# Optimization experiments

Hardware: AMD Instinct MI355X
Metric: run time of the kernel (lower is better)

The kernel has to match this reference:

```python
import jax, jax.numpy as jnp
import numpy as np

RADIUS = 2
TOP_K = 4096
TEMPERATURE = 0.1
KSIZE = 2 * RADIUS + 1  # 5


def _max_pool(x, r):
    k = 2 * r + 1
    return jax.lax.reduce_window(x, -jnp.inf, jax.lax.max,
                                 (1, 1, k, k), (1, 1, 1, 1), 'SAME')


def simple_nms(scores, r):
    zeros = jnp.zeros_like(scores)
    max_mask = scores == _max_pool(scores, r)
    for _ in range(2):
        supp_mask = _max_pool(max_mask.astype(scores.dtype), r) > 0
        supp_scores = jnp.where(supp_mask, zeros, scores)
        new_max_mask = supp_scores == _max_pool(supp_scores, r)
        max_mask = max_mask | (new_max_mask & ~supp_mask)
    return jnp.where(max_mask, scores, zeros)


def _bilinear_sample(img, px, py):
    # grid_sample, mode=bilinear, padding_mode=zeros, align_corners=True.
    # img: [H, W]; px, py: pixel coords [K]
    H, W = img.shape
    x0 = jnp.floor(px); y0 = jnp.floor(py)
    wx1 = px - x0; wx0 = 1.0 - wx1
    wy1 = py - y0; wy0 = 1.0 - wy1

    def g(xf, yf):
        xi = jnp.clip(xf.astype(jnp.int32), 0, W - 1)
        yi = jnp.clip(yf.astype(jnp.int32), 0, H - 1)
        valid = (xf >= 0) & (xf <= W - 1) & (yf >= 0) & (yf <= H - 1)
        return jnp.where(valid, img[yi, xi], 0.0)

    return (wy0 * wx0 * g(x0, y0) + wy0 * wx1 * g(x0 + 1, y0)
            + wy1 * wx0 * g(x0, y0 + 1) + wy1 * wx1 * g(x0 + 1, y0 + 1))


def setup_inputs() -> dict:
    key = jax.random.key(0)
    scores_map = jax.random.uniform(key, (8, 1, 1024, 1024), dtype=jnp.float32)
    return {'scores_map': scores_map}


def reference(scores_map):
    b, c, H, W = scores_map.shape
    r = RADIUS

    scores_nograd = jax.lax.stop_gradient(scores_map)
    nms = simple_nms(scores_nograd, r)
    # zero the borders (image_size is None)
    nms = nms.at[:, :, :r, :].set(0.0)
    nms = nms.at[:, :, :, :r].set(0.0)
    nms = nms.at[:, :, -r:, :].set(0.0)
    nms = nms.at[:, :, :, -r:].set(0.0)

    # top_k > 0 branch: fixed-size selection per image
    _, idx = jax.lax.top_k(nms.reshape(b, -1), TOP_K)  # [B, K]
    rows = idx // W
    cols = idx % W

    # soft-argmax offset grid: (dx, dy) pairs, row-major over the 5x5 patch
    lin = jnp.linspace(-r, r, KSIZE, dtype=scores_map.dtype)
    gi, gj = jnp.meshgrid(lin, lin, indexing='ij')
    hw_grid = jnp.stack([gj.reshape(-1), gi.reshape(-1)], axis=-1)  # [25, 2]

    # gather 5x5 patches at keypoints (equivalent to unfold + row-index)
    oi, oj = jnp.meshgrid(jnp.arange(KSIZE), jnp.arange(KSIZE), indexing='ij')
    oi = oi.reshape(-1); oj = oj.reshape(-1)  # [25]
    padded = jnp.pad(scores_map[:, 0], ((0, 0), (r, r), (r, r)))  # zero pad like Unfold

    def gather_patches(pad_s, rr, cc):
        return pad_s[rr[:, None] + oi[None, :], cc[:, None] + oj[None, :]]  # [K, 25]

    patches = jax.vmap(gather_patches)(padded, rows, cols)  # [B, K, 25]

    max_v = jax.lax.stop_gradient(patches.max(axis=-1, keepdims=True))
    x_exp = jnp.exp((patches - max_v) / TEMPERATURE)  # [B, K, 25]
    ssum = x_exp.sum(axis=-1)  # [B, K]
    xy_residual = jnp.einsum('bkp,pc->bkc', x_exp, hw_grid) / ssum[..., None]

    diff = (hw_grid[None, None, :, :] - xy_residual[:, :, None, :]) / r
    hw_grid_dist2 = jnp.sum(diff * diff, axis=-1)  # [B, K, 25]
    scoredispersity = jnp.sum(x_exp * hw_grid_dist2, axis=-1) / ssum  # [B, K]

    kpts_nms = jnp.stack([cols, rows], axis=-1).astype(scores_map.dtype)  # (x, y)
    wh = jnp.array([W - 1, H - 1], dtype=scores_map.dtype)
    keypoints_xy = (kpts_nms + xy_residual) / wh * 2.0 - 1.0  # [B, K, 2] in [-1, 1]

    # grid_sample lookup of the (differentiable) score map at sub-pixel locations
    px = (keypoints_xy[..., 0] + 1.0) * 0.5 * (W - 1)
    py = (keypoints_xy[..., 1] + 1.0) * 0.5 * (H - 1)
    kptscores = jax.vmap(_bilinear_sample)(scores_map[:, 0], px, py)  # [B, K]

    return keypoints_xy, scoredispersity, kptscores
```

## Files before the change

kernel.cpp:

```cpp
#include <hip/hip_runtime.h>

typedef unsigned int u32;
typedef unsigned long long u64;

#define B 8
#define H 1024
#define W 1024
#define TOPK 4096
#define CANDCAP 131072
#define GCAP 8192
#define LBUFW 320
#define CSTR 32
#define NB2 8192
#define HPAD 8200
#define BAND 4096

#define MAX5R(A, j) fmaxf(fmaxf(fmaxf(A[j], A[(j)+1]), fmaxf(A[(j)+2], A[(j)+3])), A[(j)+4])
#define OR5(A, j) (A[j] | A[(j)+1] | A[(j)+2] | A[(j)+3] | A[(j)+4])

__device__ __forceinline__ u32 bkt(u32 vb) {
    if (vb < 0x3F000000u) return 0u;
    u32 b = ((vb - 0x3F000000u) >> 10) + 1u;
    return b > NB2 ? NB2 : b;
}

__device__ __forceinline__ u64 xdilate(u64 m) {
    return m | (m << 1) | (m >> 1) | (m << 2) | (m >> 2);
}

__device__ __forceinline__ float xmax5(float v) {
    float a = fmaxf(fmaxf(__shfl_up(v, 1), __shfl_down(v, 1)), v);
    return fmaxf(a, fmaxf(__shfl_up(v, 2), __shfl_down(v, 2)));
}

__device__ __forceinline__ float selz(u64 m, float v) {
    float r;
    asm("v_cndmask_b32 %0, %1, 0, %2" : "=v"(r) : "v"(v), "s"(m));
    return r;
}
__device__ __forceinline__ float selnz(u64 m, float v) {
    float r;
    asm("v_cndmask_b32 %0, 0, %1, %2" : "=v"(r) : "v"(v), "s"(m));
    return r;
}


__global__ __launch_bounds__(256, 4) void k_nms(const float* __restrict__ S_,
                                                u64* __restrict__ cand,
                                                u32* __restrict__ cnt) {
    __shared__ u64 lbuf[4][LBUFW];

    int lane = threadIdx.x & 63;
    int wslot = threadIdx.x >> 6;
    int sx = blockIdx.x * 4 + wslot;
    int sy = blockIdx.y;
    int img = blockIdx.z;
    int gx0 = sx * 44 - 10;
    int gy0 = sy * 32;
    int gx = gx0 + lane;
    bool lxok = (unsigned)gx < (unsigned)W;
    u64 lanebit = 1ull << lane;
    const float* Sb = S_ + ((size_t)img << 20);

    u64 validx = __ballot(lxok);
    u64 emask = __ballot(lane >= 10 && lane <= 53 && gx >= 2 && gx <= W - 3);

    float S[14], R0[8], R1[8], R2[8], nxt[4];
    u64 M0[8], M1[8], SP1[6], SP2[6];
#pragma unroll
    for (int k = 0; k < 14; ++k) S[k] = -1.0f;
#pragma unroll
    for (int k = 0; k < 8; ++k) { R0[k] = -1e30f; R1[k] = -1e30f; R2[k] = -1e30f; M0[k] = 0; M1[k] = 0; }
#pragma unroll
    for (int k = 0; k < 6; ++k) { SP1[k] = 0; SP2[k] = 0; }

    u32 wbase = 0;
    int y0 = gy0 - 10;

#pragma unroll
    for (int j = 0; j < 4; ++j) {
        int gy = y0 + j;
        nxt[j] = ((unsigned)gy < (unsigned)H && lxok) ? Sb[(gy << 10) + gx] : -1.0f;
    }

    for (int cy = 0; cy < 13; ++cy, y0 += 4) {
#pragma unroll
        for (int j = 0; j < 4; ++j) S[10 + j] = nxt[j];
        if (cy < 12) {
#pragma unroll
            for (int j = 0; j < 4; ++j) {
                int gy = y0 + 4 + j;
                nxt[j] = ((unsigned)gy < (unsigned)H && lxok) ? Sb[(gy << 10) + gx] : -1.0f;
            }
        }
#pragma unroll
        for (int j = 0; j < 4; ++j) {
            R0[4 + j] = xmax5(S[10 + j]);
            float c0 = MAX5R(R0, j);
            u64 m0 = __ballot(S[j + 8] == c0) & validx;
            M0[4 + j] = m0;

            u64 sp1 = xdilate(OR5(M0, j));
            SP1[2 + j] = sp1;

            float ss1 = selz(sp1, S[j + 6]);
            R1[4 + j] = xmax5(ss1);
            float c1 = MAX5R(R1, j);
            float ss1b = selz(SP1[j], S[j + 4]);
            u64 new1 = __ballot(ss1b == c1) & validx;
            u64 m1 = M0[j] | (new1 & ~SP1[j]);
            M1[4 + j] = m1;

            u64 sp2 = xdilate(OR5(M1, j));
            SP2[2 + j] = sp2;

            float ss2 = selz(sp2, S[j + 2]);
            R2[4 + j] = xmax5(ss2);

            if (cy >= 5) {
                float c2 = MAX5R(R2, j);
                float ss2b = selz(SP2[j], S[j]);
                u64 new2 = __ballot(ss2b == c2) & validx;
                u64 m2 = M1[j] | (new2 & ~SP2[j]);
                int gy_out = y0 + j - 10;
                if (gy_out >= 2 && gy_out <= H - 3) {
                    float val = selnz(m2, S[j]);
                    u64 bm = __ballot(val > 0.0f) & emask;
                    if (bm) {
                        u32 cw = (u32)__popcll(bm);
                        u32 prefix = (u32)__popcll(bm & (lanebit - 1ull));
                        if ((bm & lanebit) && (wbase + prefix) < LBUFW) {
                            u64 key = (((u64)__float_as_uint(val)) << 32) |
                                      (u32)(~(u32)((gy_out << 10) + gx));
                            lbuf[wslot][wbase + prefix] = key;
                        }
                        wbase += cw;
                    }
                }
            }
        }
#pragma unroll
        for (int k = 0; k < 10; ++k) S[k] = S[k + 4];
#pragma unroll
        for (int k = 0; k < 4; ++k) {
            R0[k] = R0[k + 4]; R1[k] = R1[k + 4]; R2[k] = R2[k + 4];
            M0[k] = M0[k + 4]; M1[k] = M1[k + 4];
        }
#pragma unroll
        for (int k = 0; k < 2; ++k) { SP1[k] = SP1[k + 4]; SP2[k] = SP2[k + 4]; }
    }

    u32 total = wbase > LBUFW ? LBUFW : wbase;
    u32 gbase = 0;
    if (lane == 0) gbase = atomicAdd(&cnt[img * CSTR], total);
    gbase = (u32)__shfl((int)gbase, 0, 64);
    u64* dst = cand + ((size_t)img << 17);
    for (u32 i = lane; i < total; i += 64)
        dst[gbase + i] = lbuf[wslot][i];
}


__global__ __launch_bounds__(256) void k_hist(const u64* __restrict__ cand,
                                              const u32* __restrict__ cnt,
                                              u32* __restrict__ hist) {
    __shared__ u32 h[NB2 + 1];
    int img = blockIdx.y;
    int t = threadIdx.x;
    for (int i = t; i <= NB2; i += 256) h[i] = 0;
    __syncthreads();
    u32 n = cnt[img * CSTR];
    if (n > CANDCAP) n = CANDCAP;
    const u64* c = cand + ((size_t)img << 17);
    u32 per = (n + gridDim.x - 1) / gridDim.x;
    u32 lo = blockIdx.x * per;
    u32 hiX = lo + per; if (hiX > n) hiX = n;
    for (u32 i = lo + t; i < hiX; i += 256)
        atomicAdd(&h[bkt((u32)(c[i] >> 32))], 1u);
    __syncthreads();
    u32* gh = hist + (u32)img * HPAD;
    for (int i = t; i <= NB2; i += 256)
        if (h[i]) atomicAdd(&gh[i], h[i]);
}


__global__ __launch_bounds__(1024) void k_scan(const u32* __restrict__ hist,
                                               u32* __restrict__ dparr,
                                               u32* __restrict__ dpcnt,
                                               u32* __restrict__ Bsr,
                                               u32* __restrict__ gtot) {
    __shared__ u32 wpart[16], woff[16];
    __shared__ u32 sBs, sGc;
    int img = blockIdx.x, t = threadIdx.x;
    int lane = t & 63, wid = t >> 6;
    const u32* h = hist + (u32)img * HPAD;
    int hi = NB2 - 8 * t;
    u32 loc[8];
    u32 psum = 0;
#pragma unroll
    for (int i = 0; i < 8; ++i) { loc[i] = h[hi - i]; psum += loc[i]; }
    u32 incl = psum;
#pragma unroll
    for (int d = 1; d < 64; d <<= 1) {
        u32 x = (u32)__shfl_up((int)incl, d);
        if (lane >= d) incl += x;
    }
    if (lane == 63) wpart[wid] = incl;
    if (t == 0) { sBs = 0; sGc = 0; }
    __syncthreads();
    if (t == 0) { u32 a = 0; for (int w2 = 0; w2 < 16; ++w2) { woff[w2] = a; a += wpart[w2]; } }
    __syncthreads();
    u32 total1 = woff[15] + wpart[15];
    u32 excl = incl - psum + woff[wid];

    u32* dpi = dparr + (u32)img * HPAD;
    u32* dci = dpcnt + (u32)img * HPAD;
    u32 dpv = excl;
#pragma unroll
    for (int i = 0; i < 8; ++i) {
        dpi[hi - i] = dpv;
        dci[hi - i] = dpv;
        dpv += loc[i];
    }
    if (t == 1023) { dpi[0] = dpv; dci[0] = dpv; }
    if (excl < TOPK && excl + psum >= TOPK) {
        u32 cum = excl;
#pragma unroll
        for (int i = 0; i < 8; ++i) {
            cum += loc[i];
            if (cum >= TOPK) { sBs = (u32)(hi - i); sGc = cum; break; }
        }
    }
    __syncthreads();
    if (t == 0) {
        u32 bs = sBs, gc = sGc;
        if (total1 < TOPK) { bs = 0; gc = total1 + h[0]; }
        Bsr[img * CSTR] = bs;
        gtot[img * CSTR] = gc > GCAP ? GCAP : gc;
    }
}


__global__ __launch_bounds__(256) void k_gather(const u64* __restrict__ cand,
                                                const u32* __restrict__ cnt,
                                                const u32* __restrict__ Bsr,
                                                u32* __restrict__ dpcnt,
                                                u64* __restrict__ gath) {
    __shared__ u32 hb[BAND];
    __shared__ u32 ho[BAND];
    int img = blockIdx.y, t = threadIdx.x;
    for (int i = t; i < BAND; i += 256) hb[i] = 0;
    __syncthreads();
    u32 n = cnt[img * CSTR];
    if (n > CANDCAP) n = CANDCAP;
    u32 Bs = Bsr[img * CSTR];
    const u64* c = cand + ((size_t)img << 17);
    u32* dci = dpcnt + (u32)img * HPAD;
    u32 per = (n + gridDim.x - 1) / gridDim.x;
    u32 lo = blockIdx.x * per;
    u32 hiX = lo + per; if (hiX > n) hiX = n;

    for (u32 i = lo + t; i < hiX; i += 256) {
        u32 b = bkt((u32)(c[i] >> 32));
        if (b >= Bs) {
            u32 idx = b - Bs;
            if (idx < BAND) atomicAdd(&hb[idx], 1u);
        }
    }
    __syncthreads();
    for (int i = t; i < BAND; i += 256) {
        u32 cv = hb[i];
        if (cv) { ho[i] = atomicAdd(&dci[Bs + i], cv); hb[i] = 0; }
    }
    __syncthreads();
    u64* g = gath + ((size_t)img << 13);
    for (u32 i = lo + t; i < hiX; i += 256) {
        u64 key = c[i];
        u32 b = bkt((u32)(key >> 32));
        if (b < Bs) continue;
        u32 idx = b - Bs;
        u32 pos;
        if (idx < BAND) pos = ho[idx] + atomicAdd(&hb[idx], 1u);
        else pos = atomicAdd(&dci[b], 1u);
        if (pos < GCAP) g[pos] = key;
    }
}


__global__ __launch_bounds__(256) void k_rankfinal(const u64* __restrict__ gath,
                                                   const u32* __restrict__ gtot,
                                                   const u32* __restrict__ dparr,
                                                   const float* __restrict__ S,
                                                   float* __restrict__ out) {
    int img = blockIdx.y;
    u32 n = gtot[img * CSTR];
    if (n > GCAP) n = GCAP;
    u32 i = blockIdx.x * 256 + threadIdx.x;
    if (i >= n) return;
    const u64* g = gath + ((size_t)img << 13);
    u64 key = g[i];
    u32 b = bkt((u32)(key >> 32));
    const u32* dpi = dparr + (u32)img * HPAD;
    u32 lo = dpi[b];
    u32 hiE = (b >= 1) ? dpi[b - 1] : n;
    if (hiE > n) hiE = n;
    u32 r = lo;
    for (u32 j = lo; j < hiE; ++j) r += (g[j] > key);
    if (r >= TOPK) return;

    u32 rem = ~(u32)(key & 0xFFFFFFFFull);
    int row = (int)(rem >> 10);
    int col = (int)(rem & (W - 1));
    const float* Sb = S + ((size_t)img << 20);

    float p[25];
    float mx = -1e30f;
#pragma unroll
    for (int a2 = 0; a2 < 5; ++a2) {
        int y = row + a2 - 2;
#pragma unroll
        for (int c2 = 0; c2 < 5; ++c2) {
            int x = col + c2 - 2;
            float v = (y >= 0 && y < H && x >= 0 && x < W) ? Sb[(y << 10) + x] : 0.0f;
            p[a2 * 5 + c2] = v;
            mx = fmaxf(mx, v);
        }
    }
    float sum = 0.0f, sx = 0.0f, sy = 0.0f;
#pragma unroll
    for (int a2 = 0; a2 < 5; ++a2) {
#pragma unroll
        for (int c2 = 0; c2 < 5; ++c2) {
            float e = expf((p[a2 * 5 + c2] - mx) / 0.1f);
            p[a2 * 5 + c2] = e;
            sum += e;
            sx += e * (float)(c2 - 2);
            sy += e * (float)(a2 - 2);
        }
    }
    float rx = sx / sum, ry = sy / sum;
    float sd = 0.0f;
#pragma unroll
    for (int a2 = 0; a2 < 5; ++a2) {
#pragma unroll
        for (int c2 = 0; c2 < 5; ++c2) {
            float dxx = ((float)(c2 - 2) - rx) * 0.5f;
            float dyy = ((float)(a2 - 2) - ry) * 0.5f;
            sd += p[a2 * 5 + c2] * (dxx * dxx + dyy * dyy);
        }
    }
    float disp = sd / sum;
    float kx = ((float)col + rx) / (float)(W - 1) * 2.0f - 1.0f;
    float ky = ((float)row + ry) / (float)(H - 1) * 2.0f - 1.0f;

    float px = (kx + 1.0f) * 0.5f * (float)(W - 1);
    float py = (ky + 1.0f) * 0.5f * (float)(H - 1);
    float x0 = floorf(px), y0 = floorf(py);
    float wx1 = px - x0, wx0 = 1.0f - wx1;
    float wy1 = py - y0, wy0 = 1.0f - wy1;

    float gg[4];
    float xs[4] = {x0, x0 + 1.0f, x0, x0 + 1.0f};
    float ys[4] = {y0, y0, y0 + 1.0f, y0 + 1.0f};
#pragma unroll
    for (int q = 0; q < 4; ++q) {
        int xi = (int)xs[q]; xi = xi < 0 ? 0 : (xi > W - 1 ? W - 1 : xi);
        int yi = (int)ys[q]; yi = yi < 0 ? 0 : (yi > H - 1 ? H - 1 : yi);
        bool valid = (xs[q] >= 0.0f) && (xs[q] <= (float)(W - 1)) &&
                     (ys[q] >= 0.0f) && (ys[q] <= (float)(H - 1));
        gg[q] = valid ? Sb[(yi << 10) + xi] : 0.0f;
    }
    float score = wy0 * wx0 * gg[0] + wy0 * wx1 * gg[1] + wy1 * wx0 * gg[2] + wy1 * wx1 * gg[3];

    u32 slot = ((u32)img << 12) + r;
    out[(size_t)slot * 2]     = kx;
    out[(size_t)slot * 2 + 1] = ky;
    out[B * TOPK * 2 + slot]            = disp;
    out[B * TOPK * 2 + B * TOPK + slot] = score;
}


extern "C" void kernel_launch(void* const* d_in, const int* in_sizes, int n_in,
                              void* d_out, int out_size, void* d_ws, size_t ws_size,
                              hipStream_t stream) {
    const float* S = (const float*)d_in[0];
    float* out = (float*)d_out;

    char* w = (char*)d_ws;
    u64* cand = (u64*)w;        w += (size_t)B * CANDCAP * 8;
    u64* gath = (u64*)w;        w += (size_t)B * GCAP * 8;
    u32* hist = (u32*)w;        w += (size_t)B * HPAD * 4;
    u32* cnt = (u32*)w;         w += B * CSTR * 4;
    u32* dparr = (u32*)w;       w += (size_t)B * HPAD * 4;
    u32* dpcnt = (u32*)w;       w += (size_t)B * HPAD * 4;
    u32* Bsr = (u32*)w;         w += B * CSTR * 4;
    u32* gtot = (u32*)w;        w += B * CSTR * 4;

    hipMemsetAsync(hist, 0, (size_t)B * HPAD * 4 + B * CSTR * 4, stream);

    k_nms<<<dim3(6, 32, B), 256, 0, stream>>>(S, cand, cnt);
    k_hist<<<dim3(16, B), 256, 0, stream>>>(cand, cnt, hist);
    k_scan<<<B, 1024, 0, stream>>>(hist, dparr, dpcnt, Bsr, gtot);
    k_gather<<<dim3(16, B), 256, 0, stream>>>(cand, cnt, Bsr, dpcnt, gath);
    k_rankfinal<<<dim3(32, B), 256, 0, stream>>>(gath, gtot, dparr, S, out);
}
```

Before: 114.5 us.

## Fuse histogram into NMS kernel, coarsen buckets, reuse row shuffles across NMS passes

Builds the per-image score histogram inside the NMS kernel from the local candidate buffer, which removes the separate histogram kernel and its second pass over the candidate array. Bucket resolution drops from 8192 to 1024 bins, so scan, gather and shared-memory histograms get simpler and no longer need a global-atomic fallback outside the band. The horizontal max-of-5 now caches the shifted neighbour values once per row and reuses them with masked selects in the suppression passes, replacing repeated cross-lane shuffles. The cost is more registers in the NMS kernel, a shared histogram plus a barrier there, and coarser buckets that may pass more candidates into the threshold band.

```diff
diff --git a/kernel.cpp b/kernel.cpp
--- a/kernel.cpp
+++ b/kernel.cpp
@@ -11,26 +11,24 @@
 #define GCAP 8192
 #define LBUFW 320
 #define CSTR 32
-#define NB2 8192
-#define HPAD 8200
-#define BAND 4096
+#define NB 1024
+#define HPAD 1056
 
 #define MAX5R(A, j) fmaxf(fmaxf(fmaxf(A[j], A[(j)+1]), fmaxf(A[(j)+2], A[(j)+3])), A[(j)+4])
 #define OR5(A, j) (A[j] | A[(j)+1] | A[(j)+2] | A[(j)+3] | A[(j)+4])
 
 __device__ __forceinline__ u32 bkt(u32 vb) {
     if (vb < 0x3F000000u) return 0u;
-    u32 b = ((vb - 0x3F000000u) >> 10) + 1u;
-    return b > NB2 ? NB2 : b;
+    u32 b = ((vb - 0x3F000000u) >> 13) + 1u;
+    return b > NB ? NB : b;
+}
+
+__device__ __forceinline__ float max5(float a, float b, float c, float d, float e) {
+    return fmaxf(fmaxf(fmaxf(a, b), fmaxf(c, d)), e);
 }
 
 __device__ __forceinline__ u64 xdilate(u64 m) {
     return m | (m << 1) | (m >> 1) | (m << 2) | (m >> 2);
-}
-
-__device__ __forceinline__ float xmax5(float v) {
-    float a = fmaxf(fmaxf(__shfl_up(v, 1), __shfl_down(v, 1)), v);
-    return fmaxf(a, fmaxf(__shfl_up(v, 2), __shfl_down(v, 2)));
 }
 
 __device__ __forceinline__ float selz(u64 m, float v) {
@@ -47,8 +45,10 @@
 
 __global__ __launch_bounds__(256, 4) void k_nms(const float* __restrict__ S_,
                                                 u64* __restrict__ cand,
-                                                u32* __restrict__ cnt) {
+                                                u32* __restrict__ cnt,
+                                                u32* __restrict__ hist) {
     __shared__ u64 lbuf[4][LBUFW];
+    __shared__ u32 bh[NB + 1];
 
     int lane = threadIdx.x & 63;
     int wslot = threadIdx.x >> 6;
@@ -62,13 +62,17 @@
     u64 lanebit = 1ull << lane;
     const float* Sb = S_ + ((size_t)img << 20);
 
+    for (int i = threadIdx.x; i <= NB; i += 256) bh[i] = 0;
+
     u64 validx = __ballot(lxok);
     u64 emask = __ballot(lane >= 10 && lane <= 53 && gx >= 2 && gx <= W - 3);
 
-    float S[14], R0[8], R1[8], R2[8], nxt[4];
+    float S[14], U1[12], U2[12], D1[12], D2[12], R0[8], R1[8], R2[8], nxt[4];
     u64 M0[8], M1[8], SP1[6], SP2[6];
 #pragma unroll
     for (int k = 0; k < 14; ++k) S[k] = -1.0f;
+#pragma unroll
+    for (int k = 0; k < 12; ++k) { U1[k] = -1.0f; U2[k] = -1.0f; D1[k] = -1.0f; D2[k] = -1.0f; }
 #pragma unroll
     for (int k = 0; k < 8; ++k) { R0[k] = -1e30f; R1[k] = -1e30f; R2[k] = -1e30f; M0[k] = 0; M1[k] = 0; }
 #pragma unroll
@@ -95,7 +99,13 @@
         }
 #pragma unroll
         for (int j = 0; j < 4; ++j) {
-            R0[4 + j] = xmax5(S[10 + j]);
+            float v = S[10 + j];
+            U1[8 + j] = __shfl_up(v, 1);
+            U2[8 + j] = __shfl_up(v, 2);
+            D1[8 + j] = __shfl_down(v, 1);
+            D2[8 + j] = __shfl_down(v, 2);
+
+            R0[4 + j] = max5(U2[8 + j], U1[8 + j], v, D1[8 + j], D2[8 + j]);
             float c0 = MAX5R(R0, j);
             u64 m0 = __ballot(S[j + 8] == c0) & validx;
             M0[4 + j] = m0;
@@ -103,8 +113,10 @@
             u64 sp1 = xdilate(OR5(M0, j));
             SP1[2 + j] = sp1;
 
-            float ss1 = selz(sp1, S[j + 6]);
-            R1[4 + j] = xmax5(ss1);
+            float h1 = max5(selz(sp1 << 2, U2[j + 4]), selz(sp1 << 1, U1[j + 4]),
+                            selz(sp1, S[j + 6]),
+                            selz(sp1 >> 1, D1[j + 4]), selz(sp1 >> 2, D2[j + 4]));
+            R1[4 + j] = h1;
             float c1 = MAX5R(R1, j);
             float ss1b = selz(SP1[j], S[j + 4]);
             u64 new1 = __ballot(ss1b == c1) & validx;
@@ -114,8 +126,10 @@
             u64 sp2 = xdilate(OR5(M1, j));
             SP2[2 + j] = sp2;
 
-            float ss2 = selz(sp2, S[j + 2]);
-            R2[4 + j] = xmax5(ss2);
+            float h2 = max5(selz(sp2 << 2, U2[j]), selz(sp2 << 1, U1[j]),
+                            selz(sp2, S[j + 2]),
+                            selz(sp2 >> 1, D1[j]), selz(sp2 >> 2, D2[j]));
+            R2[4 + j] = h2;
 
             if (cy >= 5) {
                 float c2 = MAX5R(R2, j);
@@ -142,6 +156,8 @@
 #pragma unroll
         for (int k = 0; k < 10; ++k) S[k] = S[k + 4];
 #pragma unroll
+        for (int k = 0; k < 8; ++k) { U1[k] = U1[k + 4]; U2[k] = U2[k + 4]; D1[k] = D1[k + 4]; D2[k] = D2[k + 4]; }
+#pragma unroll
         for (int k = 0; k < 4; ++k) {
             R0[k] = R0[k + 4]; R1[k] = R1[k + 4]; R2[k] = R2[k + 4];
             M0[k] = M0[k + 4]; M1[k] = M1[k + 4];
@@ -155,31 +171,15 @@
     if (lane == 0) gbase = atomicAdd(&cnt[img * CSTR], total);
     gbase = (u32)__shfl((int)gbase, 0, 64);
     u64* dst = cand + ((size_t)img << 17);
-    for (u32 i = lane; i < total; i += 64)
-        dst[gbase + i] = lbuf[wslot][i];
-}
-
-
-__global__ __launch_bounds__(256) void k_hist(const u64* __restrict__ cand,
-                                              const u32* __restrict__ cnt,
-                                              u32* __restrict__ hist) {
-    __shared__ u32 h[NB2 + 1];
-    int img = blockIdx.y;
-    int t = threadIdx.x;
-    for (int i = t; i <= NB2; i += 256) h[i] = 0;
-    __syncthreads();
-    u32 n = cnt[img * CSTR];
-    if (n > CANDCAP) n = CANDCAP;
-    const u64* c = cand + ((size_t)img << 17);
-    u32 per = (n + gridDim.x - 1) / gridDim.x;
-    u32 lo = blockIdx.x * per;
-    u32 hiX = lo + per; if (hiX > n) hiX = n;
-    for (u32 i = lo + t; i < hiX; i += 256)
-        atomicAdd(&h[bkt((u32)(c[i] >> 32))], 1u);
+    for (u32 i = lane; i < total; i += 64) {
+        u64 key = lbuf[wslot][i];
+        dst[gbase + i] = key;
+        atomicAdd(&bh[bkt((u32)(key >> 32))], 1u);
+    }
     __syncthreads();
     u32* gh = hist + (u32)img * HPAD;
-    for (int i = t; i <= NB2; i += 256)
-        if (h[i]) atomicAdd(&gh[i], h[i]);
+    for (int i = threadIdx.x; i <= NB; i += 256)
+        if (bh[i]) atomicAdd(&gh[i], bh[i]);
 }
 
 
@@ -193,12 +193,8 @@
     int img = blockIdx.x, t = threadIdx.x;
     int lane = t & 63, wid = t >> 6;
     const u32* h = hist + (u32)img * HPAD;
-    int hi = NB2 - 8 * t;
-    u32 loc[8];
-    u32 psum = 0;
-#pragma unroll
-    for (int i = 0; i < 8; ++i) { loc[i] = h[hi - i]; psum += loc[i]; }
-    u32 incl = psum;
+    u32 v = h[NB - t];
+    u32 incl = v;
 #pragma unroll
     for (int d = 1; d < 64; d <<= 1) {
         u32 x = (u32)__shfl_up((int)incl, d);
@@ -209,31 +205,19 @@
     __syncthreads();
     if (t == 0) { u32 a = 0; for (int w2 = 0; w2 < 16; ++w2) { woff[w2] = a; a += wpart[w2]; } }
     __syncthreads();
-    u32 total1 = woff[15] + wpart[15];
-    u32 excl = incl - psum + woff[wid];
-
+    u32 cum = incl + woff[wid];
+    u32 total = woff[15] + wpart[15];
+    u32 dp = cum - v;
     u32* dpi = dparr + (u32)img * HPAD;
     u32* dci = dpcnt + (u32)img * HPAD;
-    u32 dpv = excl;
-#pragma unroll
-    for (int i = 0; i < 8; ++i) {
-        dpi[hi - i] = dpv;
-        dci[hi - i] = dpv;
-        dpv += loc[i];
-    }
-    if (t == 1023) { dpi[0] = dpv; dci[0] = dpv; }
-    if (excl < TOPK && excl + psum >= TOPK) {
-        u32 cum = excl;
-#pragma unroll
-        for (int i = 0; i < 8; ++i) {
-            cum += loc[i];
-            if (cum >= TOPK) { sBs = (u32)(hi - i); sGc = cum; break; }
-        }
-    }
+    dpi[NB - t] = dp;
+    dci[NB - t] = dp;
+    if (t == 1023) { dpi[0] = cum; dci[0] = cum; }
+    if (total >= TOPK && dp < TOPK && cum >= TOPK) { sBs = (u32)(NB - t); sGc = cum; }
     __syncthreads();
     if (t == 0) {
         u32 bs = sBs, gc = sGc;
-        if (total1 < TOPK) { bs = 0; gc = total1 + h[0]; }
+        if (total < TOPK) { bs = 0; gc = total + h[0]; }
         Bsr[img * CSTR] = bs;
         gtot[img * CSTR] = gc > GCAP ? GCAP : gc;
     }
@@ -245,10 +229,10 @@
                                                 const u32* __restrict__ Bsr,
                                                 u32* __restrict__ dpcnt,
                                                 u64* __restrict__ gath) {
-    __shared__ u32 hb[BAND];
-    __shared__ u32 ho[BAND];
+    __shared__ u32 hb[NB + 1];
+    __shared__ u32 ho[NB + 1];
     int img = blockIdx.y, t = threadIdx.x;
-    for (int i = t; i < BAND; i += 256) hb[i] = 0;
+    for (int i = t; i <= NB; i += 256) hb[i] = 0;
     __syncthreads();
     u32 n = cnt[img * CSTR];
     if (n > CANDCAP) n = CANDCAP;
@@ -261,13 +245,10 @@
 
     for (u32 i = lo + t; i < hiX; i += 256) {
         u32 b = bkt((u32)(c[i] >> 32));
-        if (b >= Bs) {
-            u32 idx = b - Bs;
-            if (idx < BAND) atomicAdd(&hb[idx], 1u);
-        }
-    }
-    __syncthreads();
-    for (int i = t; i < BAND; i += 256) {
+        if (b >= Bs) atomicAdd(&hb[b - Bs], 1u);
+    }
+    __syncthreads();
+    for (int i = t; i <= NB; i += 256) {
         u32 cv = hb[i];
         if (cv) { ho[i] = atomicAdd(&dci[Bs + i], cv); hb[i] = 0; }
     }
@@ -278,9 +259,7 @@
         u32 b = bkt((u32)(key >> 32));
         if (b < Bs) continue;
         u32 idx = b - Bs;
-        u32 pos;
-        if (idx < BAND) pos = ho[idx] + atomicAdd(&hb[idx], 1u);
-        else pos = atomicAdd(&dci[b], 1u);
+        u32 pos = ho[idx] + atomicAdd(&hb[idx], 1u);
         if (pos < GCAP) g[pos] = key;
     }
 }
@@ -397,8 +376,7 @@
 
     hipMemsetAsync(hist, 0, (size_t)B * HPAD * 4 + B * CSTR * 4, stream);
 
-    k_nms<<<dim3(6, 32, B), 256, 0, stream>>>(S, cand, cnt);
-    k_hist<<<dim3(16, B), 256, 0, stream>>>(cand, cnt, hist);
+    k_nms<<<dim3(6, 32, B), 256, 0, stream>>>(S, cand, cnt, hist);
     k_scan<<<B, 1024, 0, stream>>>(hist, dparr, dpcnt, Bsr, gtot);
     k_gather<<<dim3(16, B), 256, 0, stream>>>(cand, cnt, Bsr, dpcnt, gath);
     k_rankfinal<<<dim3(32, B), 256, 0, stream>>>(gath, gtot, dparr, S, out);
```

New measurement: 151.8 us. 1.33x slower.
